# Performance work log

Measured on AMD Instinct MI355X. Metric: run time of the kernel, lower is better.

## Reference

```python
import jax, jax.numpy as jnp
import numpy as np
from functools import partial

H = 64  # hidden_size
F = 5   # num_features
ALPHA_RANK = 1.0
NEG_SLOPE = 0.2


def setup_inputs() -> dict:
    key = jax.random.key(0)
    ks = jax.random.split(key, 10)
    N, T = 4096, 512
    feature = jax.random.normal(ks[0], (N, T, F), dtype=jnp.float32)
    ret = jax.random.normal(ks[1], (N,), dtype=jnp.float32)
    mask = jax.random.bernoulli(ks[2], 0.9, (N,))
    s = 1.0 / np.sqrt(H)
    Wih = jax.random.uniform(ks[3], (4 * H, F), jnp.float32, -s, s)
    Whh = jax.random.uniform(ks[4], (4 * H, H), jnp.float32, -s, s)
    bih = jax.random.uniform(ks[5], (4 * H,), jnp.float32, -s, s)
    bhh = jax.random.uniform(ks[6], (4 * H,), jnp.float32, -s, s)
    Wd = jax.random.uniform(ks[7], (1, H), jnp.float32, -s, s)
    bd = jax.random.uniform(ks[8], (1,), jnp.float32, -s, s)
    return {"feature": feature, "ret": ret, "mask": mask,
            "Wih": Wih, "Whh": Whh, "bih": bih, "bhh": bhh,
            "Wd": Wd, "bd": bd}


def _lstm_last_h(x, Wih, Whh, bih, bhh):
    # x: [N, T, F] -> last hidden state [N, H]. PyTorch gate order: i, f, g, o.
    N = x.shape[0]
    b = bih + bhh
    # precompute input projections for all steps: [T, N, 4H]
    x_proj = jnp.einsum('ntf,gf->tng', x, Wih) + b

    def step(carry, xt):
        h, c = carry
        gates = xt + h @ Whh.T  # [N, 4H]
        i, f, g, o = jnp.split(gates, 4, axis=-1)
        i = jax.nn.sigmoid(i)
        f = jax.nn.sigmoid(f)
        g = jnp.tanh(g)
        o = jax.nn.sigmoid(o)
        c = f * c + i * g
        h = o * jnp.tanh(c)
        return (h, c), None

    h0 = jnp.zeros((N, H), x.dtype)
    c0 = jnp.zeros((N, H), x.dtype)
    (h, _), _ = jax.lax.scan(step, (h0, c0), x_proj)
    return h


def _masked_mse(pred, gt, mask):
    m = mask.astype(pred.dtype)
    return jnp.sum((pred - gt) ** 2 * m) / (jnp.sum(m) + 1e-8)


def _rank_loss(pred, gt, mask):
    m = mask.astype(pred.dtype)
    pred_diff = pred[None, :] - pred[:, None]   # [i,j] = pred[j]-pred[i]
    true_diff = gt[None, :] - gt[:, None]
    mm = m[None, :] * m[:, None]
    return jnp.mean(jax.nn.relu(-pred_diff * true_diff * mm))


def reference(feature, ret, mask, Wih, Whh, bih, bhh, Wd, bd):
    h_last = _lstm_last_h(feature, Wih, Whh, bih, bhh)          # [N, H]
    pred = jax.nn.leaky_relu(h_last @ Wd.T + bd, NEG_SLOPE)[:, 0]  # [N]
    reg_loss = _masked_mse(pred, ret, mask)
    rank_loss = _rank_loss(pred, ret, mask)
    loss = reg_loss + ALPHA_RANK * rank_loss
    return pred, loss, reg_loss, rank_loss
```

## Files before the change

### kernel.cpp

```cpp
#include <hip/hip_runtime.h>

#define NSEQ   4096
#define TSTEPS 512
#define FIN    5
#define HID    64
#define SPB    16
#define BLK    256

typedef __attribute__((ext_vector_type(8))) short bsh8;
typedef __attribute__((ext_vector_type(4))) float f32x4;

#define MFMA16(A, B, C) __builtin_amdgcn_mfma_f32_16x16x32_bf16((A), (B), (C), 0, 0, 0)

struct Frag2 { bsh8 hi; bsh8 lo; };

__device__ __forceinline__ unsigned short bf16hi_rn(float x) {
    unsigned u = __float_as_uint(x);
    return (unsigned short)((u + 0x7fffu + ((u >> 16) & 1u)) >> 16);
}
__device__ __forceinline__ void split_bf16(float v, unsigned short& h, unsigned short& l) {
    h = bf16hi_rn(v);
    float hf = __uint_as_float(((unsigned)h) << 16);
    l = bf16hi_rn(v - hf);
}

__device__ __forceinline__ float fast_sigmoid(float x) {
    return __builtin_amdgcn_rcpf(1.0f + __expf(-x));
}
__device__ __forceinline__ float fast_tanh(float x) {
    return 1.0f - 2.0f * __builtin_amdgcn_rcpf(1.0f + __expf(2.0f * x));
}

__device__ __forceinline__ Frag2 load_whh_frag(const float* __restrict__ Whh, int gate, int k) {
    const float* p = Whh + gate * HID + k;
    Frag2 r;
#pragma unroll
    for (int j = 0; j < 8; ++j) {
        unsigned short h, l;
        split_bf16(p[j], h, l);
        r.hi[j] = (short)h; r.lo[j] = (short)l;
    }
    return r;
}
__device__ __forceinline__ Frag2 load_wih_frag(const float* __restrict__ Wih, int gate, int quad) {
    Frag2 r;
#pragma unroll
    for (int j = 0; j < 8; ++j) { r.hi[j] = 0; r.lo[j] = 0; }
    if (quad == 0) {
#pragma unroll
        for (int j = 0; j < FIN; ++j) {
            unsigned short h, l;
            split_bf16(Wih[gate * FIN + j], h, l);
            r.hi[j] = (short)h; r.lo[j] = (short)l;
        }
    }
    return r;
}

__device__ __forceinline__ void stage_chunk(const float* __restrict__ feat,
                                            bsh8 (*dst)[SPB],
                                            int seq0, int t0, int tid) {
#pragma unroll
    for (int it = 0; it < (64 * SPB) / BLK; ++it) {
        int idx = tid + it * BLK;
        int t2  = idx >> 4;
        int s   = idx & 15;
        const float* xp = feat + (size_t)(seq0 + s) * (TSTEPS * FIN) + (t0 + t2) * FIN;
        bsh8 v = {0, 0, 0, 0, 0, 0, 0, 0};
#pragma unroll
        for (int j = 0; j < FIN; ++j) v[j] = (short)bf16hi_rn(xp[j]);
        dst[t2][s] = v;
    }
}

__global__ __launch_bounds__(BLK)
void lstm_kernel(const float* __restrict__ feat,
                 const float* __restrict__ Wih,
                 const float* __restrict__ Whh,
                 const float* __restrict__ bih,
                 const float* __restrict__ bhh,
                 const float* __restrict__ Wd,
                 const float* __restrict__ bd,
                 float* __restrict__ pred,
                 float* __restrict__ accums) {
    __shared__ bsh8  aA[2][SPB][9];
    __shared__ bsh8  xb[2][64][SPB];
    __shared__ float hf[SPB][HID + 1];
    __shared__ float pf[SPB][17];

    const int tid  = threadIdx.x;
    const int w    = tid >> 6;
    const int lane = tid & 63;
    const int col  = lane & 15;
    const int quad = lane >> 4;
    const int u    = 16 * w + col;
    const int seq0 = blockIdx.x * SPB;

    if (blockIdx.x == 0 && tid < 4) accums[tid] = 0.0f;

    const int g0 = 0 * HID + u, g1 = 1 * HID + u, g2 = 2 * HID + u, g3 = 3 * HID + u;
    Frag2 b00 = load_whh_frag(Whh, g0, quad * 8);
    Frag2 b01 = load_whh_frag(Whh, g0, 32 + quad * 8);
    Frag2 b02 = load_wih_frag(Wih, g0, quad);
    Frag2 b10 = load_whh_frag(Whh, g1, quad * 8);
    Frag2 b11 = load_whh_frag(Whh, g1, 32 + quad * 8);
    Frag2 b12 = load_wih_frag(Wih, g1, quad);
    Frag2 b20 = load_whh_frag(Whh, g2, quad * 8);
    Frag2 b21 = load_whh_frag(Whh, g2, 32 + quad * 8);
    Frag2 b22 = load_wih_frag(Wih, g2, quad);
    Frag2 b30 = load_whh_frag(Whh, g3, quad * 8);
    Frag2 b31 = load_whh_frag(Whh, g3, 32 + quad * 8);
    Frag2 b32 = load_wih_frag(Wih, g3, quad);

    const float bi  = bih[g0] + bhh[g0];
    const float bf_ = bih[g1] + bhh[g1];
    const float bg  = bih[g2] + bhh[g2];
    const float bo  = bih[g3] + bhh[g3];

    {
        bsh8 z = {0, 0, 0, 0, 0, 0, 0, 0};
        if (tid < SPB * 9) (&aA[0][0][0])[tid] = z;
    }
    stage_chunk(feat, xb[0], seq0, 0, tid);
    __syncthreads();

    f32x4 acc0 = {bi,  bi,  bi,  bi };
    f32x4 acc1 = {bf_, bf_, bf_, bf_};
    f32x4 acc2 = {bg,  bg,  bg,  bg };
    f32x4 acc3 = {bo,  bo,  bo,  bo };
    {
        bsh8 ax = xb[0][0][col];
        acc0 = MFMA16(ax, b02.hi, acc0); acc0 = MFMA16(ax, b02.lo, acc0);
        acc1 = MFMA16(ax, b12.hi, acc1); acc1 = MFMA16(ax, b12.lo, acc1);
        acc2 = MFMA16(ax, b22.hi, acc2); acc2 = MFMA16(ax, b22.lo, acc2);
        acc3 = MFMA16(ax, b32.hi, acc3); acc3 = MFMA16(ax, b32.lo, acc3);
    }

    float c_[4] = {0.f, 0.f, 0.f, 0.f};

    for (int t = 0; t < TSTEPS; ++t) {
        const int tt  = t & 63;
        const int buf = t & 1;
        const int nb  = buf ^ 1;
        __syncthreads();

        if (tt == 0 && t + 64 < TSTEPS) {
            int nc = (t >> 6) + 1;
            stage_chunk(feat, xb[nc & 1], seq0, nc * 64, tid);
        }

        bsh8 ah0 = aA[buf][col][quad];
        bsh8 ah1 = aA[buf][col][4 + quad];
        acc0 = MFMA16(ah0, b00.hi, acc0); acc0 = MFMA16(ah1, b01.hi, acc0);
        acc1 = MFMA16(ah0, b10.hi, acc1); acc1 = MFMA16(ah1, b11.hi, acc1);
        acc2 = MFMA16(ah0, b20.hi, acc2); acc2 = MFMA16(ah1, b21.hi, acc2);
        acc3 = MFMA16(ah0, b30.hi, acc3); acc3 = MFMA16(ah1, b31.hi, acc3);
        acc0 = MFMA16(ah0, b00.lo, acc0); acc0 = MFMA16(ah1, b01.lo, acc0);
        acc1 = MFMA16(ah0, b10.lo, acc1); acc1 = MFMA16(ah1, b11.lo, acc1);
        acc2 = MFMA16(ah0, b20.lo, acc2); acc2 = MFMA16(ah1, b21.lo, acc2);
        acc3 = MFMA16(ah0, b30.lo, acc3); acc3 = MFMA16(ah1, b31.lo, acc3);

#pragma unroll
        for (int r = 0; r < 4; ++r) {
            float gi = fast_sigmoid(acc0[r]);
            float gf = fast_sigmoid(acc1[r]);
            float gg = fast_tanh  (acc2[r]);
            float go = fast_sigmoid(acc3[r]);
            c_[r] = gf * c_[r] + gi * gg;
            float hh = go * fast_tanh(c_[r]);
            int seqr = quad * 4 + r;
            ((unsigned short*)&aA[nb][seqr][0])[u] = bf16hi_rn(hh);
            if (t == TSTEPS - 1) hf[seqr][u] = hh;
        }

        if (t < TSTEPS - 1) {
            int t1 = t + 1;
            bsh8 ax = xb[(t1 >> 6) & 1][t1 & 63][col];
            acc0 = (f32x4){bi,  bi,  bi,  bi };
            acc1 = (f32x4){bf_, bf_, bf_, bf_};
            acc2 = (f32x4){bg,  bg,  bg,  bg };
            acc3 = (f32x4){bo,  bo,  bo,  bo };
            acc0 = MFMA16(ax, b02.hi, acc0); acc0 = MFMA16(ax, b02.lo, acc0);
            acc1 = MFMA16(ax, b12.hi, acc1); acc1 = MFMA16(ax, b12.lo, acc1);
            acc2 = MFMA16(ax, b22.hi, acc2); acc2 = MFMA16(ax, b22.lo, acc2);
            acc3 = MFMA16(ax, b32.hi, acc3); acc3 = MFMA16(ax, b32.lo, acc3);
        }
    }
    __syncthreads();

    {
        int s  = tid & 15;
        int q4 = tid >> 4;
        int j0 = q4 * 4;
        float part = hf[s][j0] * Wd[j0] + hf[s][j0 + 1] * Wd[j0 + 1]
                   + hf[s][j0 + 2] * Wd[j0 + 2] + hf[s][j0 + 3] * Wd[j0 + 3];
        pf[s][q4] = part;
    }
    __syncthreads();
    if (tid < SPB) {
        float sum = bd[0];
#pragma unroll
        for (int j = 0; j < 16; ++j) sum += pf[tid][j];
        float p = (sum >= 0.0f) ? sum : 0.2f * sum;
        pred[seq0 + tid] = p;
    }
}

__global__ __launch_bounds__(256)
void loss_kernel(const float* __restrict__ pred,
                 const float* __restrict__ ret,
                 const int* __restrict__ mask,
                 float* __restrict__ accums) {
    __shared__ float sp[NSEQ];
    __shared__ float sg[NSEQ];
    __shared__ float sq[NSEQ];
    int tid = threadIdx.x;
    for (int idx = tid; idx < NSEQ; idx += 256) {
        sp[idx] = pred[idx];
        sg[idx] = ret[idx];
        sq[idx] = (mask[idx] != 0) ? 1.0f : 0.0f;
    }
    __syncthreads();

    if (blockIdx.x == 0) {
        float v = 0.0f, m = 0.0f;
        for (int j = tid; j < NSEQ; j += 256) {
            float mj = sq[j];
            float d  = sp[j] - sg[j];
            v += d * d * mj;
            m += mj;
        }
#pragma unroll
        for (int off = 32; off > 0; off >>= 1) {
            v += __shfl_down(v, off, 64);
            m += __shfl_down(m, off, 64);
        }
        if ((tid & 63) == 0) {
            atomicAdd(&accums[0], v);
            atomicAdd(&accums[1], m);
        }
    }

    int iloc = tid >> 4;
    int jp   = tid & 15;
    int i    = blockIdx.x * 16 + iloc;
    float pi = sp[i], gi = sg[i], qi = sq[i];
    float sum = 0.0f;
    for (int j = jp; j < NSEQ; j += 16) {
        float t = -(sp[j] - pi) * (sg[j] - gi);
        sum += fmaxf(t, 0.0f) * sq[j];
    }
    sum *= qi;
#pragma unroll
    for (int off = 32; off > 0; off >>= 1) sum += __shfl_down(sum, off, 64);
    __shared__ float wsum[4];
    if ((tid & 63) == 0) wsum[tid >> 6] = sum;
    __syncthreads();
    if (tid == 0) atomicAdd(&accums[2], wsum[0] + wsum[1] + wsum[2] + wsum[3]);
}

__global__ void final_kernel(const float* __restrict__ accums,
                             float* __restrict__ out) {
    float reg  = accums[0] / (accums[1] + 1e-8f);
    float rank = accums[2] / 16777216.0f;
    out[NSEQ + 0] = reg + rank;
    out[NSEQ + 1] = reg;
    out[NSEQ + 2] = rank;
}

extern "C" void kernel_launch(void* const* d_in, const int* in_sizes, int n_in,
                              void* d_out, int out_size, void* d_ws, size_t ws_size,
                              hipStream_t stream) {
    const float* feat = (const float*)d_in[0];
    const float* ret  = (const float*)d_in[1];
    const int*   mask = (const int*)d_in[2];
    const float* Wih  = (const float*)d_in[3];
    const float* Whh  = (const float*)d_in[4];
    const float* bih  = (const float*)d_in[5];
    const float* bhh  = (const float*)d_in[6];
    const float* Wd   = (const float*)d_in[7];
    const float* bd   = (const float*)d_in[8];
    float* out    = (float*)d_out;
    float* accums = (float*)d_ws;

    lstm_kernel<<<NSEQ / SPB, BLK, 0, stream>>>(feat, Wih, Whh, bih, bhh,
                                                Wd, bd, out, accums);
    loss_kernel<<<NSEQ / 16, 256, 0, stream>>>(out, ret, mask, accums);
    final_kernel<<<1, 1, 0, stream>>>(accums, out);
}
```

Measured before the change: 399.3 us.

## Split LSTM block into recurrent and input-projection warp groups, fold activation scaling

The LSTM block doubles to 512 threads. Four waves run the recurrent Whh MFMAs and gate math at raised priority, while four producer waves stage features and compute the input projection one step ahead into a double-buffered shared seed. The bias is folded into the Wih fragment through a constant-one input lane, and the log2e sigmoid/tanh scaling is pre-multiplied into the weights so the activations use exp2 directly. The hidden state is packed with v_cvt_pk_bf16, and the loss kernel gets vectorised shared loads with 8 rows per block. The cost is more shared memory and an extra shared-memory round trip for the seeds each step, and the pre-scaling adds bf16 split-rounding risk.

```diff
diff --git a/kernel.cpp b/kernel.cpp
--- a/kernel.cpp
+++ b/kernel.cpp
@@ -5,12 +5,17 @@
 #define FIN    5
 #define HID    64
 #define SPB    16
-#define BLK    256
+#define BLK    512
 
 typedef __attribute__((ext_vector_type(8))) short bsh8;
 typedef __attribute__((ext_vector_type(4))) float f32x4;
+typedef __attribute__((ext_vector_type(4))) int   i32x4;
 
 #define MFMA16(A, B, C) __builtin_amdgcn_mfma_f32_16x16x32_bf16((A), (B), (C), 0, 0, 0)
+
+#define LOG2E 1.4426950408889634f
+#define SNEG  (-LOG2E)
+#define SPOS  (2.0f * LOG2E)
 
 struct Frag2 { bsh8 hi; bsh8 lo; };
 
@@ -20,55 +25,57 @@
 }
 __device__ __forceinline__ void split_bf16(float v, unsigned short& h, unsigned short& l) {
     h = bf16hi_rn(v);
-    float hf = __uint_as_float(((unsigned)h) << 16);
-    l = bf16hi_rn(v - hf);
-}
-
-__device__ __forceinline__ float fast_sigmoid(float x) {
-    return __builtin_amdgcn_rcpf(1.0f + __expf(-x));
-}
-__device__ __forceinline__ float fast_tanh(float x) {
-    return 1.0f - 2.0f * __builtin_amdgcn_rcpf(1.0f + __expf(2.0f * x));
-}
-
-__device__ __forceinline__ Frag2 load_whh_frag(const float* __restrict__ Whh, int gate, int k) {
-    const float* p = Whh + gate * HID + k;
+    float hf_ = __uint_as_float(((unsigned)h) << 16);
+    l = bf16hi_rn(v - hf_);
+}
+__device__ __forceinline__ float rcp1pexp2(float x) {
+    return __builtin_amdgcn_rcpf(1.0f + __builtin_amdgcn_exp2f(x));
+}
+
+__device__ __forceinline__ Frag2 load_whh_frag(const float* __restrict__ Whh, int row, int k, float scale) {
+    const float* p = Whh + row * HID + k;
     Frag2 r;
 #pragma unroll
     for (int j = 0; j < 8; ++j) {
         unsigned short h, l;
-        split_bf16(p[j], h, l);
+        split_bf16(scale * p[j], h, l);
         r.hi[j] = (short)h; r.lo[j] = (short)l;
     }
     return r;
 }
-__device__ __forceinline__ Frag2 load_wih_frag(const float* __restrict__ Wih, int gate, int quad) {
+__device__ __forceinline__ Frag2 load_wih_frag(const float* __restrict__ Wih,
+                                               const float* __restrict__ bih,
+                                               const float* __restrict__ bhh,
+                                               int row, int quad, float scale) {
     Frag2 r;
 #pragma unroll
     for (int j = 0; j < 8; ++j) { r.hi[j] = 0; r.lo[j] = 0; }
     if (quad == 0) {
+        unsigned short h, l;
 #pragma unroll
         for (int j = 0; j < FIN; ++j) {
-            unsigned short h, l;
-            split_bf16(Wih[gate * FIN + j], h, l);
+            split_bf16(scale * Wih[row * FIN + j], h, l);
             r.hi[j] = (short)h; r.lo[j] = (short)l;
         }
+        split_bf16(scale * (bih[row] + bhh[row]), h, l);
+        r.hi[FIN] = (short)h; r.lo[FIN] = (short)l;
     }
     return r;
 }
 
 __device__ __forceinline__ void stage_chunk(const float* __restrict__ feat,
                                             bsh8 (*dst)[SPB],
-                                            int seq0, int t0, int tid) {
-#pragma unroll
-    for (int it = 0; it < (64 * SPB) / BLK; ++it) {
-        int idx = tid + it * BLK;
+                                            int seq0, int t0, int tidE) {
+#pragma unroll
+    for (int it = 0; it < (64 * SPB) / 256; ++it) {
+        int idx = tidE + it * 256;
         int t2  = idx >> 4;
         int s   = idx & 15;
         const float* xp = feat + (size_t)(seq0 + s) * (TSTEPS * FIN) + (t0 + t2) * FIN;
         bsh8 v = {0, 0, 0, 0, 0, 0, 0, 0};
 #pragma unroll
         for (int j = 0; j < FIN; ++j) v[j] = (short)bf16hi_rn(xp[j]);
+        v[FIN] = (short)0x3F80;
         dst[t2][s] = v;
     }
 }
@@ -85,116 +92,141 @@
                  float* __restrict__ accums) {
     __shared__ bsh8  aA[2][SPB][9];
     __shared__ bsh8  xb[2][64][SPB];
+    __shared__ __align__(16) float seedb[2][4][HID][SPB];
     __shared__ float hf[SPB][HID + 1];
     __shared__ float pf[SPB][17];
 
-    const int tid  = threadIdx.x;
-    const int w    = tid >> 6;
-    const int lane = tid & 63;
-    const int col  = lane & 15;
-    const int quad = lane >> 4;
-    const int u    = 16 * w + col;
-    const int seq0 = blockIdx.x * SPB;
+    const int tid   = threadIdx.x;
+    const int w     = tid >> 6;
+    const int lane  = tid & 63;
+    const int col   = lane & 15;
+    const int quad  = lane >> 4;
+    const int quad4 = quad * 4;
+    const int seq0  = blockIdx.x * SPB;
 
     if (blockIdx.x == 0 && tid < 4) accums[tid] = 0.0f;
-
-    const int g0 = 0 * HID + u, g1 = 1 * HID + u, g2 = 2 * HID + u, g3 = 3 * HID + u;
-    Frag2 b00 = load_whh_frag(Whh, g0, quad * 8);
-    Frag2 b01 = load_whh_frag(Whh, g0, 32 + quad * 8);
-    Frag2 b02 = load_wih_frag(Wih, g0, quad);
-    Frag2 b10 = load_whh_frag(Whh, g1, quad * 8);
-    Frag2 b11 = load_whh_frag(Whh, g1, 32 + quad * 8);
-    Frag2 b12 = load_wih_frag(Wih, g1, quad);
-    Frag2 b20 = load_whh_frag(Whh, g2, quad * 8);
-    Frag2 b21 = load_whh_frag(Whh, g2, 32 + quad * 8);
-    Frag2 b22 = load_wih_frag(Wih, g2, quad);
-    Frag2 b30 = load_whh_frag(Whh, g3, quad * 8);
-    Frag2 b31 = load_whh_frag(Whh, g3, 32 + quad * 8);
-    Frag2 b32 = load_wih_frag(Wih, g3, quad);
-
-    const float bi  = bih[g0] + bhh[g0];
-    const float bf_ = bih[g1] + bhh[g1];
-    const float bg  = bih[g2] + bhh[g2];
-    const float bo  = bih[g3] + bhh[g3];
 
     {
         bsh8 z = {0, 0, 0, 0, 0, 0, 0, 0};
         if (tid < SPB * 9) (&aA[0][0][0])[tid] = z;
     }
-    stage_chunk(feat, xb[0], seq0, 0, tid);
-    __syncthreads();
-
-    f32x4 acc0 = {bi,  bi,  bi,  bi };
-    f32x4 acc1 = {bf_, bf_, bf_, bf_};
-    f32x4 acc2 = {bg,  bg,  bg,  bg };
-    f32x4 acc3 = {bo,  bo,  bo,  bo };
-    {
-        bsh8 ax = xb[0][0][col];
-        acc0 = MFMA16(ax, b02.hi, acc0); acc0 = MFMA16(ax, b02.lo, acc0);
-        acc1 = MFMA16(ax, b12.hi, acc1); acc1 = MFMA16(ax, b12.lo, acc1);
-        acc2 = MFMA16(ax, b22.hi, acc2); acc2 = MFMA16(ax, b22.lo, acc2);
-        acc3 = MFMA16(ax, b32.hi, acc3); acc3 = MFMA16(ax, b32.lo, acc3);
-    }
-
-    float c_[4] = {0.f, 0.f, 0.f, 0.f};
-
-    for (int t = 0; t < TSTEPS; ++t) {
-        const int tt  = t & 63;
-        const int buf = t & 1;
-        const int nb  = buf ^ 1;
-        __syncthreads();
-
-        if (tt == 0 && t + 64 < TSTEPS) {
-            int nc = (t >> 6) + 1;
-            stage_chunk(feat, xb[nc & 1], seq0, nc * 64, tid);
-        }
-
-        bsh8 ah0 = aA[buf][col][quad];
-        bsh8 ah1 = aA[buf][col][4 + quad];
-        acc0 = MFMA16(ah0, b00.hi, acc0); acc0 = MFMA16(ah1, b01.hi, acc0);
-        acc1 = MFMA16(ah0, b10.hi, acc1); acc1 = MFMA16(ah1, b11.hi, acc1);
-        acc2 = MFMA16(ah0, b20.hi, acc2); acc2 = MFMA16(ah1, b21.hi, acc2);
-        acc3 = MFMA16(ah0, b30.hi, acc3); acc3 = MFMA16(ah1, b31.hi, acc3);
-        acc0 = MFMA16(ah0, b00.lo, acc0); acc0 = MFMA16(ah1, b01.lo, acc0);
-        acc1 = MFMA16(ah0, b10.lo, acc1); acc1 = MFMA16(ah1, b11.lo, acc1);
-        acc2 = MFMA16(ah0, b20.lo, acc2); acc2 = MFMA16(ah1, b21.lo, acc2);
-        acc3 = MFMA16(ah0, b30.lo, acc3); acc3 = MFMA16(ah1, b31.lo, acc3);
-
-#pragma unroll
-        for (int r = 0; r < 4; ++r) {
-            float gi = fast_sigmoid(acc0[r]);
-            float gf = fast_sigmoid(acc1[r]);
-            float gg = fast_tanh  (acc2[r]);
-            float go = fast_sigmoid(acc3[r]);
-            c_[r] = gf * c_[r] + gi * gg;
-            float hh = go * fast_tanh(c_[r]);
-            int seqr = quad * 4 + r;
-            ((unsigned short*)&aA[nb][seqr][0])[u] = bf16hi_rn(hh);
-            if (t == TSTEPS - 1) hf[seqr][u] = hh;
-        }
-
-        if (t < TSTEPS - 1) {
-            int t1 = t + 1;
-            bsh8 ax = xb[(t1 >> 6) & 1][t1 & 63][col];
-            acc0 = (f32x4){bi,  bi,  bi,  bi };
-            acc1 = (f32x4){bf_, bf_, bf_, bf_};
-            acc2 = (f32x4){bg,  bg,  bg,  bg };
-            acc3 = (f32x4){bo,  bo,  bo,  bo };
-            acc0 = MFMA16(ax, b02.hi, acc0); acc0 = MFMA16(ax, b02.lo, acc0);
-            acc1 = MFMA16(ax, b12.hi, acc1); acc1 = MFMA16(ax, b12.lo, acc1);
-            acc2 = MFMA16(ax, b22.hi, acc2); acc2 = MFMA16(ax, b22.lo, acc2);
-            acc3 = MFMA16(ax, b32.hi, acc3); acc3 = MFMA16(ax, b32.lo, acc3);
-        }
-    }
-    __syncthreads();
-
-    {
+    if (w >= 4) stage_chunk(feat, xb[0], seq0, 0, tid - 256);
+    __syncthreads();
+
+    if (w < 4) {
+        const int u = 16 * w + col;
+        const Frag2 b00 = load_whh_frag(Whh, 0*HID + u,      quad*8, SNEG);
+        const Frag2 b01 = load_whh_frag(Whh, 0*HID + u, 32 + quad*8, SNEG);
+        const Frag2 b10 = load_whh_frag(Whh, 1*HID + u,      quad*8, SNEG);
+        const Frag2 b11 = load_whh_frag(Whh, 1*HID + u, 32 + quad*8, SNEG);
+        const Frag2 b20 = load_whh_frag(Whh, 2*HID + u,      quad*8, SPOS);
+        const Frag2 b21 = load_whh_frag(Whh, 2*HID + u, 32 + quad*8, SPOS);
+        const Frag2 b30 = load_whh_frag(Whh, 3*HID + u,      quad*8, SNEG);
+        const Frag2 b31 = load_whh_frag(Whh, 3*HID + u, 32 + quad*8, SNEG);
+
+        float cs_[4] = {0.f, 0.f, 0.f, 0.f};
+        __builtin_amdgcn_s_setprio(1);
+
+        for (int t = 0; t < TSTEPS; ++t) {
+            const int buf = t & 1;
+            const int nb  = buf ^ 1;
+            __syncthreads();
+
+            f32x4 acc0 = *(const f32x4*)&seedb[buf][0][u][quad4];
+            f32x4 acc1 = *(const f32x4*)&seedb[buf][1][u][quad4];
+            f32x4 acc2 = *(const f32x4*)&seedb[buf][2][u][quad4];
+            f32x4 acc3 = *(const f32x4*)&seedb[buf][3][u][quad4];
+            bsh8 ah0 = aA[buf][col][quad];
+            bsh8 ah1 = aA[buf][col][4 + quad];
+
+            acc0 = MFMA16(ah0, b00.hi, acc0); acc0 = MFMA16(ah1, b01.hi, acc0);
+            acc1 = MFMA16(ah0, b10.hi, acc1); acc1 = MFMA16(ah1, b11.hi, acc1);
+            acc2 = MFMA16(ah0, b20.hi, acc2); acc2 = MFMA16(ah1, b21.hi, acc2);
+            acc3 = MFMA16(ah0, b30.hi, acc3); acc3 = MFMA16(ah1, b31.hi, acc3);
+            acc0 = MFMA16(ah0, b00.lo, acc0); acc0 = MFMA16(ah1, b01.lo, acc0);
+            acc1 = MFMA16(ah0, b10.lo, acc1); acc1 = MFMA16(ah1, b11.lo, acc1);
+            acc2 = MFMA16(ah0, b20.lo, acc2); acc2 = MFMA16(ah1, b21.lo, acc2);
+            acc3 = MFMA16(ah0, b30.lo, acc3); acc3 = MFMA16(ah1, b31.lo, acc3);
+
+            float hh_[4];
+#pragma unroll
+            for (int r = 0; r < 4; ++r) {
+                float si  = rcp1pexp2(acc0[r]);
+                float sf  = rcp1pexp2(acc1[r]);
+                float rg  = rcp1pexp2(acc2[r]);
+                float so  = rcp1pexp2(acc3[r]);
+                float tgK = __builtin_fmaf(-2.0f * SPOS, rg, SPOS);
+                cs_[r] = __builtin_fmaf(sf, cs_[r], si * tgK);
+                float rc  = rcp1pexp2(cs_[r]);
+                float t2  = so * rc;
+                hh_[r] = __builtin_fmaf(-2.0f, t2, so);
+            }
+            unsigned pk01, pk23;
+            asm("v_cvt_pk_bf16_f32 %0, %1, %2" : "=v"(pk01) : "v"(hh_[0]), "v"(hh_[1]));
+            asm("v_cvt_pk_bf16_f32 %0, %1, %2" : "=v"(pk23) : "v"(hh_[2]), "v"(hh_[3]));
+            unsigned short* hp = (unsigned short*)&aA[nb][quad4][0] + u;
+            hp[0]   = (unsigned short)pk01;
+            hp[72]  = (unsigned short)(pk01 >> 16);
+            hp[144] = (unsigned short)pk23;
+            hp[216] = (unsigned short)(pk23 >> 16);
+            if (t == TSTEPS - 1) {
+                hf[quad4 + 0][u] = hh_[0];
+                hf[quad4 + 1][u] = hh_[1];
+                hf[quad4 + 2][u] = hh_[2];
+                hf[quad4 + 3][u] = hh_[3];
+            }
+        }
+        __builtin_amdgcn_s_setprio(0);
+    } else {
+        const int wE   = w - 4;
+        const int uE   = 16 * wE + col;
+        const int tidE = tid - 256;
+        const Frag2 w0 = load_wih_frag(Wih, bih, bhh, 0*HID + uE, quad, SNEG);
+        const Frag2 w1 = load_wih_frag(Wih, bih, bhh, 1*HID + uE, quad, SNEG);
+        const Frag2 w2 = load_wih_frag(Wih, bih, bhh, 2*HID + uE, quad, SPOS);
+        const Frag2 w3 = load_wih_frag(Wih, bih, bhh, 3*HID + uE, quad, SNEG);
+
+        {
+            bsh8 ax = xb[0][0][col];
+            f32x4 e0 = {0.f,0.f,0.f,0.f}, e1 = e0, e2 = e0, e3 = e0;
+            e0 = MFMA16(ax, w0.hi, e0); e0 = MFMA16(ax, w0.lo, e0);
+            e1 = MFMA16(ax, w1.hi, e1); e1 = MFMA16(ax, w1.lo, e1);
+            e2 = MFMA16(ax, w2.hi, e2); e2 = MFMA16(ax, w2.lo, e2);
+            e3 = MFMA16(ax, w3.hi, e3); e3 = MFMA16(ax, w3.lo, e3);
+            *(f32x4*)&seedb[0][0][uE][quad4] = e0;
+            *(f32x4*)&seedb[0][1][uE][quad4] = e1;
+            *(f32x4*)&seedb[0][2][uE][quad4] = e2;
+            *(f32x4*)&seedb[0][3][uE][quad4] = e3;
+        }
+        for (int t = 0; t < TSTEPS; ++t) {
+            __syncthreads();
+            if ((t & 63) == 0 && t + 64 < TSTEPS)
+                stage_chunk(feat, xb[((t >> 6) + 1) & 1], seq0, ((t >> 6) + 1) * 64, tidE);
+            if (t + 1 < TSTEPS) {
+                const int t1 = t + 1;
+                bsh8 ax = xb[(t1 >> 6) & 1][t1 & 63][col];
+                f32x4 e0 = {0.f,0.f,0.f,0.f}, e1 = e0, e2 = e0, e3 = e0;
+                e0 = MFMA16(ax, w0.hi, e0); e0 = MFMA16(ax, w0.lo, e0);
+                e1 = MFMA16(ax, w1.hi, e1); e1 = MFMA16(ax, w1.lo, e1);
+                e2 = MFMA16(ax, w2.hi, e2); e2 = MFMA16(ax, w2.lo, e2);
+                e3 = MFMA16(ax, w3.hi, e3); e3 = MFMA16(ax, w3.lo, e3);
+                const int sb = t1 & 1;
+                *(f32x4*)&seedb[sb][0][uE][quad4] = e0;
+                *(f32x4*)&seedb[sb][1][uE][quad4] = e1;
+                *(f32x4*)&seedb[sb][2][uE][quad4] = e2;
+                *(f32x4*)&seedb[sb][3][uE][quad4] = e3;
+            }
+        }
+    }
+    __syncthreads();
+
+    if (tid < 256) {
         int s  = tid & 15;
-        int q4 = tid >> 4;
-        int j0 = q4 * 4;
+        int hq = tid >> 4;
+        int j0 = hq * 4;
         float part = hf[s][j0] * Wd[j0] + hf[s][j0 + 1] * Wd[j0 + 1]
                    + hf[s][j0 + 2] * Wd[j0 + 2] + hf[s][j0 + 3] * Wd[j0 + 3];
-        pf[s][q4] = part;
+        pf[s][hq] = part;
     }
     __syncthreads();
     if (tid < SPB) {
@@ -211,14 +243,21 @@
                  const float* __restrict__ ret,
                  const int* __restrict__ mask,
                  float* __restrict__ accums) {
-    __shared__ float sp[NSEQ];
-    __shared__ float sg[NSEQ];
-    __shared__ float sq[NSEQ];
+    __shared__ __align__(16) float sp[NSEQ];
+    __shared__ __align__(16) float sg[NSEQ];
+    __shared__ __align__(16) float sq[NSEQ];
+    __shared__ float wsum[8];
     int tid = threadIdx.x;
-    for (int idx = tid; idx < NSEQ; idx += 256) {
-        sp[idx] = pred[idx];
-        sg[idx] = ret[idx];
-        sq[idx] = (mask[idx] != 0) ? 1.0f : 0.0f;
+    for (int idx = tid; idx < NSEQ / 4; idx += 256) {
+        f32x4 p4 = ((const f32x4*)pred)[idx];
+        f32x4 g4 = ((const f32x4*)ret)[idx];
+        i32x4 m4 = ((const i32x4*)mask)[idx];
+        f32x4 q4;
+#pragma unroll
+        for (int l = 0; l < 4; ++l) q4[l] = m4[l] ? 1.0f : 0.0f;
+        *(f32x4*)&sp[idx * 4] = p4;
+        *(f32x4*)&sg[idx * 4] = g4;
+        *(f32x4*)&sq[idx * 4] = q4;
     }
     __syncthreads();
 
@@ -241,22 +280,31 @@
         }
     }
 
-    int iloc = tid >> 4;
-    int jp   = tid & 15;
-    int i    = blockIdx.x * 16 + iloc;
+    int iloc = tid >> 5;
+    int jp   = tid & 31;
+    int i    = blockIdx.x * 8 + iloc;
     float pi = sp[i], gi = sg[i], qi = sq[i];
     float sum = 0.0f;
-    for (int j = jp; j < NSEQ; j += 16) {
-        float t = -(sp[j] - pi) * (sg[j] - gi);
-        sum += fmaxf(t, 0.0f) * sq[j];
+    for (int j0 = jp * 4; j0 < NSEQ; j0 += 128) {
+        f32x4 p4 = *(const f32x4*)&sp[j0];
+        f32x4 g4 = *(const f32x4*)&sg[j0];
+        f32x4 q4 = *(const f32x4*)&sq[j0];
+#pragma unroll
+        for (int l = 0; l < 4; ++l) {
+            float t = -(p4[l] - pi) * (g4[l] - gi);
+            sum += fmaxf(t, 0.0f) * q4[l];
+        }
     }
     sum *= qi;
 #pragma unroll
-    for (int off = 32; off > 0; off >>= 1) sum += __shfl_down(sum, off, 64);
-    __shared__ float wsum[4];
-    if ((tid & 63) == 0) wsum[tid >> 6] = sum;
-    __syncthreads();
-    if (tid == 0) atomicAdd(&accums[2], wsum[0] + wsum[1] + wsum[2] + wsum[3]);
+    for (int off = 16; off > 0; off >>= 1) sum += __shfl_down(sum, off, 32);
+    if (jp == 0) wsum[iloc] = sum;
+    __syncthreads();
+    if (tid == 0) {
+        float s = wsum[0] + wsum[1] + wsum[2] + wsum[3]
+                + wsum[4] + wsum[5] + wsum[6] + wsum[7];
+        atomicAdd(&accums[2], s);
+    }
 }
 
 __global__ void final_kernel(const float* __restrict__ accums,
@@ -285,6 +333,6 @@
 
     lstm_kernel<<<NSEQ / SPB, BLK, 0, stream>>>(feat, Wih, Whh, bih, bhh,
                                                 Wd, bd, out, accums);
-    loss_kernel<<<NSEQ / 16, 256, 0, stream>>>(out, ret, mask, accums);
+    loss_kernel<<<NSEQ / 8, 256, 0, stream>>>(out, ret, mask, accums);
     final_kernel<<<1, 1, 0, stream>>>(accums, out);
 }
```

Measured after the change: 365.6 us. 8.4% less time.
